# Optimization experiments

Measured on AMD Instinct MI355X. Metric: run time of the kernel, lower is better.

## Reference

```python
import jax, jax.numpy as jnp
import numpy as np

NEG_SLOPE = 0.01  # nn.LeakyReLU default

def _leaky(x):
    return jnp.where(x >= 0, x, NEG_SLOPE * x)

def setup_inputs() -> dict:
    key = jax.random.key(0)
    ks = jax.random.split(key, 8)
    in_ch = 64
    B, H, W = 8, 256, 256
    x = jax.random.normal(ks[0], (B, 2 * in_ch, H, W), dtype=jnp.float32)
    dims = [(64, 128), (32, 64), (16, 32), (8, 16), (4, 8), (2, 4), (1, 2)]
    inp = {"x": x}
    for i, (o, c) in enumerate(dims):
        # kaiming_normal_ fan_out, relu: std = sqrt(2 / fan_out), fan_out = o*1*1
        std = np.sqrt(2.0 / o).astype(np.float32)
        inp[f"w{i+1}"] = jax.random.normal(ks[i + 1], (o, c), dtype=jnp.float32) * std
    return inp

def reference(x, w1, w2, w3, w4, w5, w6, w7):
    # Each 1x1 conv (bias-free) is a per-pixel matmul over channels.
    h = x
    for w in (w1, w2, w3, w4, w5, w6):
        h = _leaky(jnp.einsum('bchw,oc->bohw', h, w))
    out = jnp.einsum('bchw,oc->bohw', h, w7)  # final conv, no activation
    return out
```

## Files before the change

kernel.cpp:

```cpp
#include <hip/hip_runtime.h>


#define NEG_SLOPE 0.01f
constexpr int HW = 65536;
constexpr int GRID = 512;
constexpr int TPB  = 8;
constexpr size_t TSTRIDE = (size_t)128 * HW;

typedef __attribute__((ext_vector_type(8))) short bf16x8;
typedef __attribute__((ext_vector_type(4))) float f32x4;
typedef __attribute__((ext_vector_type(2))) float f32x2;

__device__ __forceinline__ float leaky(float v) { return fmaxf(v, v * NEG_SLOPE); }

__device__ __forceinline__ unsigned pk2(float a, float b) {
    __bf16 ba = (__bf16)a, bb = (__bf16)b;
    unsigned short ua = __builtin_bit_cast(unsigned short, ba);
    unsigned short ub = __builtin_bit_cast(unsigned short, bb);
    return (unsigned)ua | ((unsigned)ub << 16);
}

__device__ __forceinline__ bf16x8 loadA(const float* __restrict__ wsrc, int C, int m, int k) {
    f32x4 lo = *(const f32x4*)(wsrc + m * C + k);
    f32x4 hi = *(const f32x4*)(wsrc + m * C + k + 4);
    union { bf16x8 v; unsigned u[4]; } r;
    r.u[0] = pk2(lo[0], lo[1]); r.u[1] = pk2(lo[2], lo[3]);
    r.u[2] = pk2(hi[0], hi[1]); r.u[3] = pk2(hi[2], hi[3]);
    return r.v;
}

__device__ __forceinline__ void async_cp16(const float* g, float* l) {
    __builtin_amdgcn_global_load_lds((const __attribute__((address_space(1))) unsigned*)g,
                                     (__attribute__((address_space(3))) unsigned*)l,
                                     16, 0, 0);
}

__device__ __forceinline__ void cfence() { asm volatile("" ::: "memory"); }

__global__ __launch_bounds__(256, 2) void fused_spread_kernel(
    const float* __restrict__ x,
    const float* __restrict__ w1, const float* __restrict__ w2,
    const float* __restrict__ w3, const float* __restrict__ w4,
    const float* __restrict__ w5, const float* __restrict__ w6,
    const float* __restrict__ w7, float* __restrict__ out) {
    __shared__ float lds_x[4][3][1024];
    __shared__ float lds_s[4][1088];
    __shared__ float lds_tw[176];

    const int tid = threadIdx.x;
    if (tid < 128)      lds_tw[tid] = w4[tid];
    else if (tid < 160) lds_tw[tid] = w5[tid - 128];
    else if (tid < 168) lds_tw[tid] = w6[tid - 160];
    else if (tid < 170) lds_tw[tid] = w7[tid - 168];

    const int w    = tid >> 6;
    const int lane = tid & 63;
    const int n    = lane & 15;
    const int q    = lane >> 4;
    const int pl   = lane & 31;
    const int half = lane >> 5;
    const int r    = lane >> 3;
    const int s4   = (lane & 7) * 4;

    const int b = blockIdx.x;
    const float* xg = x + b * 128 + w * 32;

    __syncthreads();

    bf16x8 a1[4][4];
#pragma unroll
    for (int Mt = 0; Mt < 4; ++Mt)
#pragma unroll
        for (int kc = 0; kc < 4; ++kc)
            a1[Mt][kc] = loadA(w1, 128, Mt * 16 + n, kc * 32 + q * 8);
    bf16x8 a2[2][2];
#pragma unroll
    for (int Mt = 0; Mt < 2; ++Mt)
#pragma unroll
        for (int kc = 0; kc < 2; ++kc)
            a2[Mt][kc] = loadA(w2, 64, Mt * 16 + n, kc * 32 + q * 8);
    bf16x8 a3 = loadA(w3, 32, n, q * 8);
    cfence();
    __builtin_amdgcn_sched_barrier(0);

    float* ldsw = &lds_x[w][0][0];
#define STAGE(BASE, KCX, BUF) do {                                                   \
        const float* gb_ = (BASE) + (size_t)((KCX) * 32 + r) * HW;                   \
        float* lb_ = ldsw + (BUF) * 1024;                                            \
        _Pragma("unroll")                                                            \
        for (int i_ = 0; i_ < 4; ++i_)                                               \
            async_cp16(gb_ + (size_t)(i_ * 8) * HW + (s4 ^ (i_ * 8)), lb_ + i_ * 256); \
    } while (0)

    STAGE(xg, 0, 0);
    STAGE(xg, 1, 1);
    STAGE(xg, 2, 2);
    cfence();

    const int pq = q * 8;
    int bt = 0;

    for (int it = 0; it < TPB; ++it) {
        const float* xg_it = xg + (size_t)it * TSTRIDE;
        const float* xg_nt = xg_it + TSTRIDE;
        const bool   more  = (it < TPB - 1);

        int b1 = bt + 1; if (b1 >= 3) b1 -= 3;
        int b2 = bt + 2; if (b2 >= 3) b2 -= 3;
        const int bufk[4] = {bt, b1, b2, bt};

        f32x4 acc1[4][2];
#pragma unroll
        for (int Mt = 0; Mt < 4; ++Mt)
#pragma unroll
            for (int Nt = 0; Nt < 2; ++Nt) acc1[Mt][Nt] = (f32x4){0.f, 0.f, 0.f, 0.f};

#pragma unroll
        for (int kc = 0; kc < 4; ++kc) {
            if (kc <= 1) {
                if (it == 0) asm volatile("s_waitcnt vmcnt(8)" ::: "memory");
                else         asm volatile("s_waitcnt vmcnt(9)" ::: "memory");
            } else if (kc == 2) {
                if (it == 0) asm volatile("s_waitcnt vmcnt(4)" ::: "memory");
                else         asm volatile("s_waitcnt vmcnt(5)" ::: "memory");
            } else {
                asm volatile("s_waitcnt vmcnt(0)" ::: "memory");
            }
            __builtin_amdgcn_sched_barrier(0);

            const float* xb = ldsw + bufk[kc] * 1024;
#pragma unroll
            for (int Nt = 0; Nt < 2; ++Nt) {
                const int pxsw = (Nt * 16 + n) ^ pq;
                float t[8];
#pragma unroll
                for (int j = 0; j < 8; ++j)
                    t[j] = xb[(pq + j) * 32 + pxsw];
                union { bf16x8 v; unsigned u[4]; } bb;
                bb.u[0] = pk2(t[0], t[1]); bb.u[1] = pk2(t[2], t[3]);
                bb.u[2] = pk2(t[4], t[5]); bb.u[3] = pk2(t[6], t[7]);
#pragma unroll
                for (int Mt = 0; Mt < 4; ++Mt)
                    acc1[Mt][Nt] = __builtin_amdgcn_mfma_f32_16x16x32_bf16(a1[Mt][kc], bb.v, acc1[Mt][Nt], 0, 0, 0);
            }
            __builtin_amdgcn_sched_barrier(0);

            if (kc == 0) { STAGE(xg_it, 3, bt); cfence(); }
        }

        float* Sw = &lds_s[w][0];
        short* h1 = (short*)Sw;
#pragma unroll
        for (int Mt = 0; Mt < 4; ++Mt)
#pragma unroll
            for (int Nt = 0; Nt < 2; ++Nt) {
                int px = Nt * 16 + n;
                uint2 v;
                v.x = pk2(leaky(acc1[Mt][Nt][0]), leaky(acc1[Mt][Nt][1]));
                v.y = pk2(leaky(acc1[Mt][Nt][2]), leaky(acc1[Mt][Nt][3]));
                *(uint2*)(h1 + px * 68 + Mt * 16 + q * 4) = v;
            }
        cfence();
        if (more) { STAGE(xg_nt, 0, b1); cfence(); }

        f32x4 acc2[2][2];
#pragma unroll
        for (int Mt = 0; Mt < 2; ++Mt)
#pragma unroll
            for (int Nt = 0; Nt < 2; ++Nt) acc2[Mt][Nt] = (f32x4){0.f, 0.f, 0.f, 0.f};
#pragma unroll
        for (int Nt = 0; Nt < 2; ++Nt)
#pragma unroll
            for (int kc = 0; kc < 2; ++kc) {
                int off = (Nt * 16 + n) * 68 + kc * 32 + q * 8;
                uint2 lo = *(const uint2*)(h1 + off);
                uint2 hi = *(const uint2*)(h1 + off + 4);
                union { bf16x8 v; unsigned u[4]; } bb;
                bb.u[0] = lo.x; bb.u[1] = lo.y; bb.u[2] = hi.x; bb.u[3] = hi.y;
#pragma unroll
                for (int Mt = 0; Mt < 2; ++Mt)
                    acc2[Mt][Nt] = __builtin_amdgcn_mfma_f32_16x16x32_bf16(a2[Mt][kc], bb.v, acc2[Mt][Nt], 0, 0, 0);
            }
        cfence();
        if (more) { STAGE(xg_nt, 1, b2); cfence(); }

        short* h2 = (short*)Sw;
#pragma unroll
        for (int Mt = 0; Mt < 2; ++Mt)
#pragma unroll
            for (int Nt = 0; Nt < 2; ++Nt) {
                int px = Nt * 16 + n;
                uint2 v;
                v.x = pk2(leaky(acc2[Mt][Nt][0]), leaky(acc2[Mt][Nt][1]));
                v.y = pk2(leaky(acc2[Mt][Nt][2]), leaky(acc2[Mt][Nt][3]));
                *(uint2*)(h2 + px * 36 + Mt * 16 + q * 4) = v;
            }
        cfence();

        f32x4 acc3[2];
#pragma unroll
        for (int Nt = 0; Nt < 2; ++Nt) {
            int off = (Nt * 16 + n) * 36 + q * 8;
            uint2 lo = *(const uint2*)(h2 + off);
            uint2 hi = *(const uint2*)(h2 + off + 4);
            union { bf16x8 v; unsigned u[4]; } bb;
            bb.u[0] = lo.x; bb.u[1] = lo.y; bb.u[2] = hi.x; bb.u[3] = hi.y;
            f32x4 zero = {0.f, 0.f, 0.f, 0.f};
            acc3[Nt] = __builtin_amdgcn_mfma_f32_16x16x32_bf16(a3, bb.v, zero, 0, 0, 0);
        }
        cfence();

        float* h3 = Sw;
#pragma unroll
        for (int Nt = 0; Nt < 2; ++Nt) {
            int px = Nt * 16 + n;
            f32x2 va = {leaky(acc3[Nt][0]), leaky(acc3[Nt][1])};
            f32x2 vb = {leaky(acc3[Nt][2]), leaky(acc3[Nt][3])};
            *(f32x2*)(h3 + px * 18 + q * 4)     = va;
            *(f32x2*)(h3 + px * 18 + q * 4 + 2) = vb;
        }
        cfence();
        if (more) { STAGE(xg_nt, 2, bt); cfence(); }

        float hh[8];
#pragma unroll
        for (int c = 0; c < 8; ++c) hh[c] = h3[pl * 18 + half * 8 + c];

        float g4[8];
#pragma unroll
        for (int o = 0; o < 8; ++o) {
            float a = 0.f;
#pragma unroll
            for (int c = 0; c < 8; ++c) a = fmaf(lds_tw[o * 16 + half * 8 + c], hh[c], a);
            a += __shfl_xor(a, 32, 64);
            g4[o] = leaky(a);
        }
        float g5[4];
#pragma unroll
        for (int o = 0; o < 4; ++o) {
            float a = 0.f;
#pragma unroll
            for (int c = 0; c < 4; ++c)
                a = fmaf(lds_tw[128 + o * 8 + half * 4 + c], g4[half * 4 + c], a);
            a += __shfl_xor(a, 32, 64);
            g5[o] = leaky(a);
        }
        float g6[2];
#pragma unroll
        for (int o = 0; o < 2; ++o) {
            float a = fmaf(lds_tw[160 + o * 4 + half * 2], g5[half * 2],
                           lds_tw[160 + o * 4 + half * 2 + 1] * g5[half * 2 + 1]);
            a += __shfl_xor(a, 32, 64);
            g6[o] = leaky(a);
        }
        float a7 = lds_tw[168 + half] * g6[half];
        float res = a7 + __shfl_xor(a7, 32, 64);
        if (lane < 32) out[b * 128 + it * 65536 + w * 32 + pl] = res;
        cfence();

        bt = b1;
    }
#undef STAGE
}

extern "C" void kernel_launch(void* const* d_in, const int* in_sizes, int n_in,
                              void* d_out, int out_size, void* d_ws, size_t ws_size,
                              hipStream_t stream) {
    const float* x  = (const float*)d_in[0];
    const float* w1 = (const float*)d_in[1];
    const float* w2 = (const float*)d_in[2];
    const float* w3 = (const float*)d_in[3];
    const float* w4 = (const float*)d_in[4];
    const float* w5 = (const float*)d_in[5];
    const float* w6 = (const float*)d_in[6];
    const float* w7 = (const float*)d_in[7];
    float* out = (float*)d_out;

    fused_spread_kernel<<<GRID, 256, 0, stream>>>(x, w1, w2, w3, w4, w5, w6, w7, out);
}
```

Before: 378.0 us.

## Run layers 4-6 tail on MFMA with zero-padded bf16 tiles

Replaces the scalar FMA plus cross-half shuffle implementation of layers 4-6 with padded 16x16x32 bf16 MFMAs. Intermediates go through per-wave LDS as bf16, and the weights are loaded once into registers, so the LDS weight table and the block barrier are gone. The aim is to cut VALU work and shuffles in the per-tile tail. In exchange, most of each MFMA is wasted on zero padding, several LDS round-trips and dependent MFMA stages are added, and the tail layers now round to bf16, which lowers precision.

Measured after the change: 375.2 us. About the same (-0.7%).

```diff
diff --git a/kernel.cpp b/kernel.cpp
--- a/kernel.cpp
+++ b/kernel.cpp
@@ -9,7 +9,6 @@
 
 typedef __attribute__((ext_vector_type(8))) short bf16x8;
 typedef __attribute__((ext_vector_type(4))) float f32x4;
-typedef __attribute__((ext_vector_type(2))) float f32x2;
 
 __device__ __forceinline__ float leaky(float v) { return fmaxf(v, v * NEG_SLOPE); }
 
@@ -37,7 +36,7 @@
 
 __device__ __forceinline__ void cfence() { asm volatile("" ::: "memory"); }
 
-__global__ __launch_bounds__(256, 2) void fused_spread_kernel(
+__global__ __launch_bounds__(256, 2) void fused_mfmatail_kernel(
     const float* __restrict__ x,
     const float* __restrict__ w1, const float* __restrict__ w2,
     const float* __restrict__ w3, const float* __restrict__ w4,
@@ -45,27 +44,18 @@
     const float* __restrict__ w7, float* __restrict__ out) {
     __shared__ float lds_x[4][3][1024];
     __shared__ float lds_s[4][1088];
-    __shared__ float lds_tw[176];
 
     const int tid = threadIdx.x;
-    if (tid < 128)      lds_tw[tid] = w4[tid];
-    else if (tid < 160) lds_tw[tid] = w5[tid - 128];
-    else if (tid < 168) lds_tw[tid] = w6[tid - 160];
-    else if (tid < 170) lds_tw[tid] = w7[tid - 168];
-
     const int w    = tid >> 6;
     const int lane = tid & 63;
     const int n    = lane & 15;
     const int q    = lane >> 4;
     const int pl   = lane & 31;
-    const int half = lane >> 5;
     const int r    = lane >> 3;
     const int s4   = (lane & 7) * 4;
 
     const int b = blockIdx.x;
     const float* xg = x + b * 128 + w * 32;
-
-    __syncthreads();
 
     bf16x8 a1[4][4];
 #pragma unroll
@@ -80,6 +70,21 @@
         for (int kc = 0; kc < 2; ++kc)
             a2[Mt][kc] = loadA(w2, 64, Mt * 16 + n, kc * 32 + q * 8);
     bf16x8 a3 = loadA(w3, 32, n, q * 8);
+
+    const bf16x8 zero8 = {0, 0, 0, 0, 0, 0, 0, 0};
+    bf16x8 t4 = loadA(w4, 16, n & 7, (q & 1) * 8);
+    bf16x8 a4 = (n < 8 && q < 2) ? t4 : zero8;
+    bf16x8 t5 = loadA(w5, 8, n & 3, 0);
+    bf16x8 a5 = (n < 4 && q == 0) ? t5 : zero8;
+    bf16x8 a6 = zero8;
+    {
+        f32x4 lo = *(const f32x4*)(w6 + (n & 1) * 4);
+        union { bf16x8 v; unsigned u[4]; } r6;
+        r6.u[0] = pk2(lo[0], lo[1]); r6.u[1] = pk2(lo[2], lo[3]);
+        r6.u[2] = 0; r6.u[3] = 0;
+        if (n < 2 && q == 0) a6 = r6.v;
+    }
+    const float w7a = w7[0], w7b = w7[1];
     cfence();
     __builtin_amdgcn_sched_barrier(0);
 
@@ -210,51 +215,101 @@
         }
         cfence();
 
-        float* h3 = Sw;
+        short* h3 = (short*)Sw;
 #pragma unroll
         for (int Nt = 0; Nt < 2; ++Nt) {
             int px = Nt * 16 + n;
-            f32x2 va = {leaky(acc3[Nt][0]), leaky(acc3[Nt][1])};
-            f32x2 vb = {leaky(acc3[Nt][2]), leaky(acc3[Nt][3])};
-            *(f32x2*)(h3 + px * 18 + q * 4)     = va;
-            *(f32x2*)(h3 + px * 18 + q * 4 + 2) = vb;
+            uint2 v;
+            v.x = pk2(leaky(acc3[Nt][0]), leaky(acc3[Nt][1]));
+            v.y = pk2(leaky(acc3[Nt][2]), leaky(acc3[Nt][3]));
+            *(uint2*)(h3 + px * 24 + q * 4) = v;
         }
         cfence();
         if (more) { STAGE(xg_nt, 2, bt); cfence(); }
 
-        float hh[8];
-#pragma unroll
-        for (int c = 0; c < 8; ++c) hh[c] = h3[pl * 18 + half * 8 + c];
-
-        float g4[8];
-#pragma unroll
-        for (int o = 0; o < 8; ++o) {
-            float a = 0.f;
-#pragma unroll
-            for (int c = 0; c < 8; ++c) a = fmaf(lds_tw[o * 16 + half * 8 + c], hh[c], a);
-            a += __shfl_xor(a, 32, 64);
-            g4[o] = leaky(a);
-        }
-        float g5[4];
-#pragma unroll
-        for (int o = 0; o < 4; ++o) {
-            float a = 0.f;
-#pragma unroll
-            for (int c = 0; c < 4; ++c)
-                a = fmaf(lds_tw[128 + o * 8 + half * 4 + c], g4[half * 4 + c], a);
-            a += __shfl_xor(a, 32, 64);
-            g5[o] = leaky(a);
-        }
-        float g6[2];
-#pragma unroll
-        for (int o = 0; o < 2; ++o) {
-            float a = fmaf(lds_tw[160 + o * 4 + half * 2], g5[half * 2],
-                           lds_tw[160 + o * 4 + half * 2 + 1] * g5[half * 2 + 1]);
-            a += __shfl_xor(a, 32, 64);
-            g6[o] = leaky(a);
-        }
-        float a7 = lds_tw[168 + half] * g6[half];
-        float res = a7 + __shfl_xor(a7, 32, 64);
+        f32x4 acc4[2];
+#pragma unroll
+        for (int Nt = 0; Nt < 2; ++Nt) {
+            int px = Nt * 16 + n;
+            uint4 t = *(const uint4*)(h3 + px * 24 + (q & 1) * 8);
+            union { bf16x8 v; unsigned u[4]; } bb;
+            bool z = (q >= 2);
+            bb.u[0] = z ? 0u : t.x; bb.u[1] = z ? 0u : t.y;
+            bb.u[2] = z ? 0u : t.z; bb.u[3] = z ? 0u : t.w;
+            f32x4 zero = {0.f, 0.f, 0.f, 0.f};
+            acc4[Nt] = __builtin_amdgcn_mfma_f32_16x16x32_bf16(a4, bb.v, zero, 0, 0, 0);
+        }
+        cfence();
+
+        short* h4 = (short*)Sw;
+#pragma unroll
+        for (int Nt = 0; Nt < 2; ++Nt) {
+            if (q < 2) {
+                int px = Nt * 16 + n;
+                uint2 v;
+                v.x = pk2(leaky(acc4[Nt][0]), leaky(acc4[Nt][1]));
+                v.y = pk2(leaky(acc4[Nt][2]), leaky(acc4[Nt][3]));
+                *(uint2*)(h4 + px * 12 + q * 4) = v;
+            }
+        }
+        cfence();
+
+        f32x4 acc5[2];
+#pragma unroll
+        for (int Nt = 0; Nt < 2; ++Nt) {
+            int px = Nt * 16 + n;
+            uint2 lo = *(const uint2*)(h4 + px * 12);
+            uint2 hi = *(const uint2*)(h4 + px * 12 + 4);
+            union { bf16x8 v; unsigned u[4]; } bb;
+            bool z = (q != 0);
+            bb.u[0] = z ? 0u : lo.x; bb.u[1] = z ? 0u : lo.y;
+            bb.u[2] = z ? 0u : hi.x; bb.u[3] = z ? 0u : hi.y;
+            f32x4 zero = {0.f, 0.f, 0.f, 0.f};
+            acc5[Nt] = __builtin_amdgcn_mfma_f32_16x16x32_bf16(a5, bb.v, zero, 0, 0, 0);
+        }
+        cfence();
+
+        short* h5 = (short*)Sw;
+#pragma unroll
+        for (int Nt = 0; Nt < 2; ++Nt) {
+            if (q == 0) {
+                int px = Nt * 16 + n;
+                uint2 v;
+                v.x = pk2(leaky(acc5[Nt][0]), leaky(acc5[Nt][1]));
+                v.y = pk2(leaky(acc5[Nt][2]), leaky(acc5[Nt][3]));
+                *(uint2*)(h5 + px * 8) = v;
+            }
+        }
+        cfence();
+
+        f32x4 acc6[2];
+#pragma unroll
+        for (int Nt = 0; Nt < 2; ++Nt) {
+            int px = Nt * 16 + n;
+            uint2 lo = *(const uint2*)(h5 + px * 8);
+            union { bf16x8 v; unsigned u[4]; } bb;
+            bool z = (q != 0);
+            bb.u[0] = z ? 0u : lo.x; bb.u[1] = z ? 0u : lo.y;
+            bb.u[2] = 0u; bb.u[3] = 0u;
+            f32x4 zero = {0.f, 0.f, 0.f, 0.f};
+            acc6[Nt] = __builtin_amdgcn_mfma_f32_16x16x32_bf16(a6, bb.v, zero, 0, 0, 0);
+        }
+        cfence();
+
+        short* h6 = (short*)Sw;
+#pragma unroll
+        for (int Nt = 0; Nt < 2; ++Nt) {
+            if (q == 0) {
+                int px = Nt * 16 + n;
+                *(unsigned*)(h6 + px * 2) = pk2(leaky(acc6[Nt][0]), leaky(acc6[Nt][1]));
+            }
+        }
+        cfence();
+
+        unsigned cc = *(const unsigned*)(h6 + pl * 2);
+        float c0 = __uint_as_float(cc << 16);
+        float c1 = __uint_as_float(cc & 0xffff0000u);
+        float res = fmaf(w7a, c0, w7b * c1);
         if (lane < 32) out[b * 128 + it * 65536 + w * 32 + pl] = res;
         cfence();
 
@@ -276,5 +331,5 @@
     const float* w7 = (const float*)d_in[7];
     float* out = (float*)d_out;
 
-    fused_spread_kernel<<<GRID, 256, 0, stream>>>(x, w1, w2, w3, w4, w5, w6, w7, out);
-}
+    fused_mfmatail_kernel<<<GRID, 256, 0, stream>>>(x, w1, w2, w3, w4, w5, w6, w7, out);
+}
```
